# Kernel optimization log

Measured on AMD Instinct MI355X. Metric: run time of the kernel, lower is better.

The kernel has to match this reference:

```python
import jax, jax.numpy as jnp
import numpy as np

B, N, H, HID, L = 16, 256, 1024, 300, 64


def setup_inputs() -> dict:
    key = jax.random.key(0)
    ks = jax.random.split(key, 10)
    s = 0.02
    inp = {}
    inp["input"] = jax.random.normal(ks[0], (B, N, H), jnp.float32)
    # variable-length valid-token mask (first tokens always valid)
    lengths = jax.random.randint(ks[1], (B,), N // 2, N + 1)
    inp["logits_mask"] = jnp.arange(N)[None, :] < lengths[:, None]
    inp["labels"] = jax.random.randint(ks[2], (B, N, N), 0, L)
    inp["mlp_h_W"] = jax.random.normal(ks[3], (HID, H), jnp.float32) * s
    inp["mlp_h_b"] = jnp.zeros((HID,), jnp.float32)
    inp["mlp_d_W"] = jax.random.normal(ks[4], (HID, H), jnp.float32) * s
    inp["mlp_d_b"] = jnp.zeros((HID,), jnp.float32)
    # Bilinear with bias_x=bias_y=True -> weight [L, HID+1, HID+1]
    inp["bilinear_W"] = jax.random.normal(ks[5], (L, HID + 1, HID + 1), jnp.float32) * s
    inp["start_trans"] = jax.random.normal(ks[6], (L,), jnp.float32) * 0.1
    inp["trans"] = jax.random.normal(ks[7], (L, L), jnp.float32) * 0.1
    inp["end_trans"] = jax.random.normal(ks[8], (L,), jnp.float32) * 0.1
    return inp


def reference(input, logits_mask, labels, mlp_h_W, mlp_h_b, mlp_d_W, mlp_d_b,
              bilinear_W, start_trans, trans, end_trans):
    # --- biaffine scores (dropout is identity in eval) ---
    rel_h = jax.nn.relu(input @ mlp_h_W.T + mlp_h_b)            # [B,N,HID]
    rel_d = jax.nn.relu(input @ mlp_d_W.T + mlp_d_b)            # [B,N,HID]
    ones = jnp.ones((B, N, 1), rel_h.dtype)
    h1 = jnp.concatenate([rel_h, ones], -1)                     # [B,N,HID+1]
    d1 = jnp.concatenate([rel_d, ones], -1)
    # rel_atten(rel_d, rel_h) -> [B,L,Nd,Nh]; permute -> [B,Nd,Nh,L]
    s_rel = jnp.einsum('bxi,lij,byj->bxyl', d1, bilinear_W, h1)  # [B,N,N,L]

    # --- masked flatten: instead of compacting rows (data-dependent shape),
    # keep all B*N rows and weight each row's contribution by index = mask[:,0].
    # Mathematically identical to the torch compaction. ---
    s_flat = s_rel.reshape(B * N, N, L)
    emissions = jax.nn.log_softmax(s_flat, -1)                  # [M,N,L]
    crf_mask = jnp.broadcast_to(logits_mask[:, None, :], (B, N, N)).reshape(B * N, N)
    row_w = logits_mask.reshape(-1).astype(emissions.dtype)     # index = mask[:,0]
    tags = labels.reshape(B * N, N)
    mf = crf_mask.astype(emissions.dtype)

    # --- CRF numerator (vectorized, no recurrence) ---
    emit_sc = jnp.take_along_axis(emissions, tags[..., None], -1)[..., 0]  # [M,N]
    num = start_trans[tags[:, 0]] + (emit_sc * mf).sum(-1)
    num = num + (trans[tags[:, :-1], tags[:, 1:]] * mf[:, 1:]).sum(-1)
    last_idx = crf_mask.sum(-1).astype(jnp.int32) - 1
    last_tags = jnp.take_along_axis(tags, last_idx[:, None], 1)[:, 0]
    num = num + end_trans[last_tags]

    # --- CRF partition function via scan ---
    alpha0 = start_trans[None, :] + emissions[:, 0]             # [M,L]
    e_seq = emissions[:, 1:].swapaxes(0, 1)                     # [N-1,M,L]
    m_seq = crf_mask[:, 1:].swapaxes(0, 1)                      # [N-1,M]

    def fwd_step(alpha, xs):
        e_t, m_t = xs
        nxt = jax.nn.logsumexp(alpha[:, :, None] + trans[None], axis=1) + e_t
        return jnp.where(m_t[:, None], nxt, alpha), None

    alpha, _ = jax.lax.scan(fwd_step, alpha0, (e_seq, m_seq))
    den = jax.nn.logsumexp(alpha + end_trans[None, :], -1)
    loss = -((num - den) * row_w).sum()                         # reduction='sum'

    # --- Viterbi decode (padded; frozen tag repeated past seq end) ---
    ar = jnp.arange(L)

    def vit_step(score, xs):
        e_t, m_t = xs
        sc = score[:, :, None] + trans[None]                    # [M,L_prev,L_cur]
        idx = jnp.argmax(sc, axis=1)                            # [M,L]
        nxt = jnp.max(sc, axis=1) + e_t
        hist = jnp.where(m_t[:, None], idx, ar[None, :])
        return jnp.where(m_t[:, None], nxt, score), hist

    score, hist = jax.lax.scan(vit_step, alpha0, (e_seq, m_seq))
    last = jnp.argmax(score + end_trans[None, :], -1)           # [M]

    def btk(cur, h):
        prev = jnp.take_along_axis(h, cur[:, None], 1)[:, 0]
        return prev, prev

    _, rev = jax.lax.scan(btk, last, hist, reverse=True)        # [N-1,M]
    decoded = jnp.concatenate([rev.swapaxes(0, 1), last[:, None]], axis=1)  # [M,N]
    return loss, s_flat, decoded
```

## Files before the change

### kernel.cpp

```cpp
#include <hip/hip_runtime.h>
#include <math.h>


typedef short bf16x8 __attribute__((ext_vector_type(8)));
typedef float f32x4 __attribute__((ext_vector_type(4)));

__device__ __forceinline__ float rlf(float v, int l) {
    return __uint_as_float(__builtin_amdgcn_readlane(__float_as_uint(v), (unsigned)l));
}
__device__ __forceinline__ int rli(int v, int l) {
    return __builtin_amdgcn_readlane(v, (unsigned)l);
}
__device__ __forceinline__ unsigned short f2bf(float x) {
    union { float f; unsigned u; } c; c.f = x;
    unsigned r = c.u + 0x7FFF + ((c.u >> 16) & 1);
    return (unsigned short)(r >> 16);
}
__device__ __forceinline__ float bf2f(unsigned short h) {
    union { unsigned u; float f; } c; c.u = ((unsigned)h) << 16; return c.f;
}
__device__ __forceinline__ void gload16(const void* g, const void* lds) {
    __builtin_amdgcn_global_load_lds(
        (const __attribute__((address_space(1))) void*)g,
        (__attribute__((address_space(3))) void*)lds, 16, 0, 0);
}

__global__ void mask_cvt_kernel(const void* __restrict__ mraw, int* __restrict__ maskI,
                                int* __restrict__ lenB, int* __restrict__ zbuf) {
    int b = blockIdx.x, t = threadIdx.x;
    if (b == 0 && t < 8) zbuf[t] = 0;
    int i = b * 256 + t;
    unsigned int w0 = ((const unsigned int*)mraw)[0];
    int v;
    if (w0 == 1u)               v = ((const int*)mraw)[i];
    else if (w0 == 0x3F800000u) v = (((const float*)mraw)[i] != 0.f) ? 1 : 0;
    else                        v = ((const unsigned char*)mraw)[i] ? 1 : 0;
    maskI[i] = v;
    __shared__ int sh[4];
    int s = v;
    #pragma unroll
    for (int m = 32; m; m >>= 1) s += __shfl_xor(s, m);
    if ((t & 63) == 0) sh[t >> 6] = s;
    __syncthreads();
    if (t == 0) lenB[b] = sh[0] + sh[1] + sh[2] + sh[3];
}

__global__ __launch_bounds__(256)
void wsplit_kernel(const float* __restrict__ Wbil,
                   unsigned short* __restrict__ Wbh, unsigned short* __restrict__ Wbl) {
    __shared__ float Tile[304][17];
    const int l = blockIdx.x, jt = blockIdx.y, t = threadIdx.x;
    const int j0 = jt * 16;
    {
        int jj = t & 15, it = t >> 4;
        #pragma unroll
        for (int ib = 0; ib < 19; ++ib) {
            int i = ib * 16 + it;
            float v = 0.f;
            if (i < 301 && j0 + jj < 301)
                v = Wbil[(size_t)l * 90601 + (size_t)i * 301 + j0 + jj];
            Tile[i][jj] = v;
        }
    }
    __syncthreads();
    {
        int il = t & 15, jj = t >> 4;
        #pragma unroll
        for (int ib = 0; ib < 19; ++ib) {
            int i = ib * 16 + il;
            float v = Tile[i][jj];
            unsigned short hi = f2bf(v);
            unsigned short lo = f2bf(v - bf2f(hi));
            size_t o = ((size_t)(l * 304 + j0 + jj)) * 304 + i;
            Wbh[o] = hi; Wbl[o] = lo;
        }
    }
}

__global__ __launch_bounds__(256)
void mlp_kernel(const float* __restrict__ A,
                const float* __restrict__ Wh, const float* __restrict__ bh_,
                const float* __restrict__ Wd, const float* __restrict__ bd_,
                unsigned short* __restrict__ h1h, unsigned short* __restrict__ h1l,
                unsigned short* __restrict__ d1h, unsigned short* __restrict__ d1l) {
    constexpr int BM = 128, BN = 128, BK = 16;
    __shared__ float As[BK][BM + 4];
    __shared__ float Bs[BK][BN + 4];

    const int t = threadIdx.x;
    const int tn = t & 15, tm = t >> 4;
    const size_t a_row0 = (size_t)blockIdx.x * BM;
    const int n0 = blockIdx.y * BN;
    const int z = blockIdx.z;
    const float* Bm = z ? Wd : Wh;
    const float* bias = z ? bd_ : bh_;
    unsigned short* Ch = z ? d1h : h1h;
    unsigned short* Cl = z ? d1l : h1l;

    float acc[2][2][4][4] = {};
    const int ar = t >> 2, ak = (t & 3) * 4;

    for (int k0 = 0; k0 < 1024; k0 += BK) {
        {
            const float* ap = A + (a_row0 + ar) * 1024 + k0 + ak;
            float4 v0 = *(const float4*)ap;
            float4 v1 = *(const float4*)(ap + 64 * 1024);
            As[ak + 0][ar] = v0.x; As[ak + 1][ar] = v0.y;
            As[ak + 2][ar] = v0.z; As[ak + 3][ar] = v0.w;
            As[ak + 0][64 + ar] = v1.x; As[ak + 1][64 + ar] = v1.y;
            As[ak + 2][64 + ar] = v1.z; As[ak + 3][64 + ar] = v1.w;
        }
        {
            int r1 = min(n0 + ar, 299), r2 = min(n0 + 64 + ar, 299);
            const float* q1 = Bm + (size_t)r1 * 1024 + k0 + ak;
            const float* q2 = Bm + (size_t)r2 * 1024 + k0 + ak;
            float4 v0 = *(const float4*)q1;
            float4 v1 = *(const float4*)q2;
            Bs[ak + 0][ar] = v0.x; Bs[ak + 1][ar] = v0.y;
            Bs[ak + 2][ar] = v0.z; Bs[ak + 3][ar] = v0.w;
            Bs[ak + 0][64 + ar] = v1.x; Bs[ak + 1][64 + ar] = v1.y;
            Bs[ak + 2][64 + ar] = v1.z; Bs[ak + 3][64 + ar] = v1.w;
        }
        __syncthreads();
        #pragma unroll
        for (int kk = 0; kk < BK; ++kk) {
            float4 a0 = *(const float4*)&As[kk][tm * 4];
            float4 a1 = *(const float4*)&As[kk][64 + tm * 4];
            float4 b0 = *(const float4*)&Bs[kk][tn * 4];
            float4 b1 = *(const float4*)&Bs[kk][64 + tn * 4];
            float av[2][4] = {{a0.x, a0.y, a0.z, a0.w}, {a1.x, a1.y, a1.z, a1.w}};
            float bv[2][4] = {{b0.x, b0.y, b0.z, b0.w}, {b1.x, b1.y, b1.z, b1.w}};
            #pragma unroll
            for (int ih = 0; ih < 2; ++ih)
                #pragma unroll
                for (int ii = 0; ii < 4; ++ii)
                    #pragma unroll
                    for (int jh = 0; jh < 2; ++jh)
                        #pragma unroll
                        for (int jj = 0; jj < 4; ++jj)
                            acc[ih][jh][ii][jj] =
                                fmaf(av[ih][ii], bv[jh][jj], acc[ih][jh][ii][jj]);
        }
        __syncthreads();
    }

    #pragma unroll
    for (int ih = 0; ih < 2; ++ih) {
        #pragma unroll
        for (int ii = 0; ii < 4; ++ii) {
            int r = ih * 64 + tm * 4 + ii;
            #pragma unroll
            for (int jh = 0; jh < 2; ++jh) {
                int n = n0 + jh * 64 + tn * 4;
                if (n < 304) {
                    float o[4];
                    #pragma unroll
                    for (int q = 0; q < 4; ++q) {
                        int nq = n + q;
                        float v = acc[ih][jh][ii][q];
                        o[q] = (nq < 300) ? fmaxf(v + bias[min(nq, 299)], 0.f)
                                          : ((nq == 300) ? 1.f : 0.f);
                    }
                    ushort4 h4, l4;
                    h4.x = f2bf(o[0]); l4.x = f2bf(o[0] - bf2f(h4.x));
                    h4.y = f2bf(o[1]); l4.y = f2bf(o[1] - bf2f(h4.y));
                    h4.z = f2bf(o[2]); l4.z = f2bf(o[2] - bf2f(h4.z));
                    h4.w = f2bf(o[3]); l4.w = f2bf(o[3] - bf2f(h4.w));
                    size_t base = (a_row0 + r) * 304 + n;
                    *(ushort4*)&Ch[base] = h4;
                    *(ushort4*)&Cl[base] = l4;
                }
            }
        }
    }
}

template <int MODE>
__global__ __launch_bounds__(256)
void gemm_mfma(const unsigned short* __restrict__ Ah, const unsigned short* __restrict__ Al,
               const unsigned short* __restrict__ Bh, const unsigned short* __restrict__ Bl,
               float* __restrict__ outF, unsigned short* __restrict__ outUh,
               unsigned short* __restrict__ outUl, const unsigned short* __restrict__ zbuf,
               int c0) {
    __shared__ short Als[128 * 64];
    __shared__ short Bls[128 * 64];

    const int t = threadIdx.x;
    const int lane = t & 63;
    const int w = t >> 6, wr = w >> 1, wc = w & 1;
    const int bx = blockIdx.x, n0 = blockIdx.y * 128;

    int arow0;
    if constexpr (MODE == 1) {
        arow0 = c0 * 256 + bx * 128;
    } else {
        arow0 = (c0 + blockIdx.z) * 256 + bx * 128;
    }

    int kcd[4];
    size_t rowA[4], rowB[4];
    const short* ldsA[4];
    const short* ldsB[4];
    #pragma unroll
    for (int c4 = 0; c4 < 4; ++c4) {
        int ch = c4 * 256 + t;
        int r = ch >> 3;
        kcd[c4] = (ch & 7) ^ (r & 7);
        rowA[c4] = (size_t)(arow0 + r) * 304;
        if constexpr (MODE == 1) {
            rowB[c4] = (size_t)(n0 + r) * 304;
        } else {
            int rb = n0 + r;
            rowB[c4] = (size_t)(blockIdx.z * 256 + (rb >> 6)) * 19456 +
                       (size_t)(rb & 63) * 304;
        }
        int wavebase = (c4 * 256 + (t & ~63)) * 8;
        ldsA[c4] = &Als[wavebase];
        ldsB[c4] = &Bls[wavebase];
    }

    f32x4 acc[4][4];
    #pragma unroll
    for (int i = 0; i < 4; ++i)
        #pragma unroll
        for (int j = 0; j < 4; ++j)
            acc[i][j] = (f32x4){0.f, 0.f, 0.f, 0.f};

    const int rowA_l = wr * 64 + (lane & 15);
    const int rowB_l = wc * 64 + (lane & 15);
    const int csub = lane >> 4;
    const int cxor = lane & 7;

    for (int it = 0; it < 15; ++it) {
        const int it8 = it * 8;
        #pragma unroll
        for (int c4 = 0; c4 < 4; ++c4) {
            int kg = it8 + kcd[c4];
            {
                const unsigned short* sa;
                if (kg < 38)       sa = Ah + rowA[c4] + (size_t)kg * 8;
                else if (kg < 76)  sa = Al + rowA[c4] + (size_t)(kg - 38) * 8;
                else if (kg < 114) sa = Ah + rowA[c4] + (size_t)(kg - 76) * 8;
                else               sa = zbuf;
                gload16(sa, ldsA[c4]);
            }
            {
                const unsigned short* sb;
                if (kg < 38)       sb = Bh + rowB[c4] + (size_t)kg * 8;
                else if (kg < 76)  sb = Bh + rowB[c4] + (size_t)(kg - 38) * 8;
                else if (kg < 114) sb = Bl + rowB[c4] + (size_t)(kg - 76) * 8;
                else               sb = zbuf;
                gload16(sb, ldsB[c4]);
            }
        }
        __syncthreads();

        #pragma unroll
        for (int kh = 0; kh < 2; ++kh) {
            const int kcr = ((kh * 4 + csub) ^ cxor) * 8;
            bf16x8 af[4], bfr[4];
            #pragma unroll
            for (int f = 0; f < 4; ++f)
                af[f] = *(const bf16x8*)&Als[(rowA_l + f * 16) * 64 + kcr];
            #pragma unroll
            for (int f = 0; f < 4; ++f)
                bfr[f] = *(const bf16x8*)&Bls[(rowB_l + f * 16) * 64 + kcr];
            #pragma unroll
            for (int fr = 0; fr < 4; ++fr)
                #pragma unroll
                for (int fb = 0; fb < 4; ++fb)
                    acc[fr][fb] = __builtin_amdgcn_mfma_f32_16x16x32_bf16(
                        af[fr], bfr[fb], acc[fr][fb], 0, 0, 0);
        }
        __syncthreads();
    }

    const int mbase = bx * 128 + wr * 64 + ((lane >> 4) << 2);
    const int nbase = n0 + wc * 64 + (lane & 15);
    #pragma unroll
    for (int fb = 0; fb < 4; ++fb) {
        const int n = nbase + fb * 16;
        if constexpr (MODE == 1) {
            #pragma unroll
            for (int fr = 0; fr < 4; ++fr) {
                #pragma unroll
                for (int reg = 0; reg < 4; ++reg) {
                    int xloc = mbase + fr * 16 + reg;
                    float v = acc[fr][fb][reg];
                    unsigned short hi = f2bf(v);
                    unsigned short lo = f2bf(v - bf2f(hi));
                    size_t o = (size_t)xloc * 19456 + n;
                    outUh[o] = hi;
                    outUl[o] = lo;
                }
            }
        } else {
            const int xx = n >> 6, lt = n & 63;
            const size_t sbase = (size_t)(c0 + blockIdx.z) * 4194304 +
                                 (size_t)xx * 16384 + lt;
            #pragma unroll
            for (int fr = 0; fr < 4; ++fr) {
                #pragma unroll
                for (int reg = 0; reg < 4; ++reg) {
                    int y = mbase + fr * 16 + reg;
                    outF[sbase + (size_t)y * 64] = acc[fr][fb][reg];
                }
            }
        }
    }
}

__global__ __launch_bounds__(256, 4)
void fwd_kernel(const float* __restrict__ s_flat, const int* __restrict__ lenB,
                const int* __restrict__ maskI, const int* __restrict__ labels,
                const float* __restrict__ trans, const float* __restrict__ start_trans,
                const float* __restrict__ end_trans, float* __restrict__ rowterm) {
    __shared__ float T[4096];
    const int t = threadIdx.x;
    for (int i = t; i < 4096; i += 256) T[i] = trans[i];
    __syncthreads();

    const int lane = t & 63, wid = t >> 6;
    const int row = blockIdx.x * 4 + wid;
    if (maskI[row] == 0) {
        if (lane == 0) rowterm[row] = 0.f;
        return;
    }
    const int b = row >> 8;
    const int len = lenB[b];
    const float* srow = s_flat + (size_t)row * 16384;
    const int* lrow = labels + (size_t)row * 256;

    float Ec[64];
    #pragma unroll
    for (int p = 0; p < 64; ++p) Ec[p] = __expf(T[p * 64 + lane]);

    const float et = end_trans[lane];

    float sv = srow[lane];
    int tagprev = lrow[0];
    float num = start_trans[tagprev] + rlf(sv, tagprev);
    float alpha = start_trans[lane] + sv;

    float sv_pre = srow[64 + lane];

    for (int y = 1; y < len; ++y) {
        sv = sv_pre;
        int ynext = (y + 1 < len) ? (y + 1) : (len - 1);
        sv_pre = srow[ynext * 64 + lane];

        const int tag = lrow[y];
        num += rlf(sv, tag) + T[tagprev * 64 + tag];
        tagprev = tag;

        float am = alpha;
        #pragma unroll
        for (int m = 32; m; m >>= 1) am = fmaxf(am, __shfl_xor(am, m));
        float ea = __expf(alpha - am);
        float a0 = 0.f, a1 = 0.f, a2 = 0.f, a3 = 0.f;
        #pragma unroll
        for (int p = 0; p < 64; p += 4) {
            a0 = fmaf(rlf(ea, p + 0), Ec[p + 0], a0);
            a1 = fmaf(rlf(ea, p + 1), Ec[p + 1], a1);
            a2 = fmaf(rlf(ea, p + 2), Ec[p + 2], a2);
            a3 = fmaf(rlf(ea, p + 3), Ec[p + 3], a3);
        }
        alpha = am + __logf((a0 + a1) + (a2 + a3)) + sv;
    }

    num += end_trans[tagprev];

    float da = alpha + et;
    float dmx = da;
    #pragma unroll
    for (int m = 32; m; m >>= 1) dmx = fmaxf(dmx, __shfl_xor(dmx, m));
    float ds = __expf(da - dmx);
    #pragma unroll
    for (int m = 32; m; m >>= 1) ds += __shfl_xor(ds, m);
    float den = dmx + __logf(ds);

    if (lane == 0) rowterm[row] = num - den;
}

__global__ __launch_bounds__(256, 4)
void vitf_kernel(const float* __restrict__ s_flat, const int* __restrict__ lenB,
                 const float* __restrict__ trans, const float* __restrict__ start_trans,
                 const float* __restrict__ end_trans, float* __restrict__ vsb,
                 float* __restrict__ decoded) {
    const int t = threadIdx.x;
    const int lane = t & 63, wid = t >> 6;
    const int row = blockIdx.x * 4 + wid;
    const int len = lenB[row >> 8];
    const float* srow = s_flat + (size_t)row * 16384;
    float* vrow = vsb + (size_t)row * 16384;

    float sv = srow[lane];
    float vs = start_trans[lane] + sv;
    float sv_pre = srow[64 + lane];

    for (int y = 1; y < len; ++y) {
        vrow[(y - 1) * 64 + lane] = vs;
        float svc = sv_pre;
        int ynext = (y + 1 < len) ? (y + 1) : (len - 1);
        sv_pre = srow[ynext * 64 + lane];

        float m0 = -3.4e38f, m1 = -3.4e38f, m2 = -3.4e38f, m3 = -3.4e38f;
        #pragma unroll
        for (int p = 0; p < 64; p += 8) {
            float t0 = rlf(vs, p + 0) + trans[(p + 0) * 64 + lane];
            float t1 = rlf(vs, p + 1) + trans[(p + 1) * 64 + lane];
            m0 = fmaxf(fmaxf(t0, t1), m0);
            float t2 = rlf(vs, p + 2) + trans[(p + 2) * 64 + lane];
            float t3 = rlf(vs, p + 3) + trans[(p + 3) * 64 + lane];
            m1 = fmaxf(fmaxf(t2, t3), m1);
            float t4 = rlf(vs, p + 4) + trans[(p + 4) * 64 + lane];
            float t5 = rlf(vs, p + 5) + trans[(p + 5) * 64 + lane];
            m2 = fmaxf(fmaxf(t4, t5), m2);
            float t6 = rlf(vs, p + 6) + trans[(p + 6) * 64 + lane];
            float t7 = rlf(vs, p + 7) + trans[(p + 7) * 64 + lane];
            m3 = fmaxf(fmaxf(t6, t7), m3);
        }
        vs = fmaxf(fmaxf(m0, m1), fmaxf(m2, m3)) + svc;
    }

    float fe = vs + end_trans[lane];
    float mx = fe;
    #pragma unroll
    for (int m = 32; m; m >>= 1) mx = fmaxf(mx, __shfl_xor(mx, m));
    unsigned long long msk = __ballot(fe == mx);
    int fi = (int)__builtin_ctzll(msk);

    if (lane == 0) decoded[(size_t)row * 256 + 255] = (float)fi;
}

__global__ __launch_bounds__(256)
void vitb_kernel(const float* __restrict__ vsb, const int* __restrict__ lenB,
                 const float* __restrict__ trans, float* __restrict__ decoded) {
    __shared__ float Tt[64][65];
    const int t = threadIdx.x;
    for (int i = t; i < 4096; i += 256) {
        int p = i >> 6, c = i & 63;
        Tt[c][p] = trans[i];
    }
    __syncthreads();

    const int lane = t & 63, wid = t >> 6;
    const int row = blockIdx.x * 4 + wid;
    const int len = lenB[row >> 8];
    const float* vrow = vsb + (size_t)row * 16384;
    float* drow = decoded + (size_t)row * 256;

    int cur = (int)drow[255];

    for (int y = len - 1 + lane; y < 255; y += 64) drow[y] = (float)cur;

    float v0 = vrow[(len - 2) * 64 + lane];
    float v1 = (len >= 3) ? vrow[(len - 3) * 64 + lane] : 0.f;

    for (int y = len - 2; y >= 0; --y) {
        float vy = v0;
        v0 = v1;
        v1 = (y >= 2) ? vrow[(y - 2) * 64 + lane] : 0.f;

        float tp = vy + Tt[cur][lane];
        float mx = tp;
        #pragma unroll
        for (int m = 32; m; m >>= 1) mx = fmaxf(mx, __shfl_xor(mx, m));
        unsigned long long msk = __ballot(tp == mx);
        cur = (int)__builtin_ctzll(msk);
        if (lane == 0) drow[y] = (float)cur;
    }
}

__global__ __launch_bounds__(256, 3)
void vit_kernel(const float* __restrict__ s_flat, const int* __restrict__ lenB,
                const float* __restrict__ trans, const float* __restrict__ start_trans,
                const float* __restrict__ end_trans, unsigned char* __restrict__ hist,
                float* __restrict__ decoded) {
    const int t = threadIdx.x;
    const int lane = t & 63, wid = t >> 6;
    const int row = blockIdx.x * 4 + wid;
    const int len = lenB[row >> 8];
    const float* srow = s_flat + (size_t)row * 16384;
    unsigned char* hrow = hist + (size_t)row * 16320;

    float sv = srow[lane];
    float vs = start_trans[lane] + sv;
    float sv_pre = srow[64 + lane];

    for (int y = 1; y < len; ++y) {
        sv = sv_pre;
        int ynext = (y + 1 < len) ? (y + 1) : (len - 1);
        sv_pre = srow[ynext * 64 + lane];

        float b0 = -3.4e38f, b1 = -3.4e38f, b2 = -3.4e38f, b3 = -3.4e38f;
        int i0 = 0, i1 = 1, i2 = 2, i3 = 3;
        #pragma unroll
        for (int p = 0; p < 64; p += 4) {
            float t0 = rlf(vs, p + 0) + trans[(p + 0) * 64 + lane]; if (t0 > b0) { b0 = t0; i0 = p + 0; }
            float t1 = rlf(vs, p + 1) + trans[(p + 1) * 64 + lane]; if (t1 > b1) { b1 = t1; i1 = p + 1; }
            float t2 = rlf(vs, p + 2) + trans[(p + 2) * 64 + lane]; if (t2 > b2) { b2 = t2; i2 = p + 2; }
            float t3 = rlf(vs, p + 3) + trans[(p + 3) * 64 + lane]; if (t3 > b3) { b3 = t3; i3 = p + 3; }
        }
        bool c;
        c = (b1 > b0) || (b1 == b0 && i1 < i0);
        float bA = c ? b1 : b0; int iA = c ? i1 : i0;
        c = (b3 > b2) || (b3 == b2 && i3 < i2);
        float bB = c ? b3 : b2; int iB = c ? i3 : i2;
        c = (bB > bA) || (bB == bA && iB < iA);
        float bbv = c ? bB : bA; int bi = c ? iB : iA;

        hrow[(size_t)(y - 1) * 64 + lane] = (unsigned char)bi;
        vs = bbv + sv;
    }

    float fv = vs + end_trans[lane]; int fi = lane;
    #pragma unroll
    for (int m = 32; m; m >>= 1) {
        float ov = __shfl_xor(fv, m);
        int oi = __shfl_xor(fi, m);
        bool cc = (ov > fv) || (ov == fv && oi < fi);
        fv = cc ? ov : fv; fi = cc ? oi : fi;
    }

    if (lane == 0) decoded[(size_t)row * 256 + 255] = (float)fi;
}

__global__ __launch_bounds__(256)
void backtrack_kernel(const unsigned char* __restrict__ hist, const int* __restrict__ lenB,
                      float* __restrict__ decoded) {
    const int lane = threadIdx.x & 63, wid = threadIdx.x >> 6;
    const int row = blockIdx.x * 4 + wid;
    const int len = lenB[row >> 8];
    const unsigned char* hrow = hist + (size_t)row * 16320;
    float* drow = decoded + (size_t)row * 256;

    int cur = (int)drow[255];
    for (int y = len - 1 + lane; y < 255; y += 64) drow[y] = (float)cur;

    int t0 = len - 2;
    int c0 = (int)hrow[(t0 - 0) * 64 + lane];
    int c1 = (int)hrow[(t0 - 1) * 64 + lane];
    int c2 = (int)hrow[(t0 - 2) * 64 + lane];
    int c3 = (int)hrow[(t0 - 3) * 64 + lane];

    for (int y = t0; y >= 0; y -= 4) {
        int yn = y - 4;
        int n0 = 0, n1 = 0, n2 = 0, n3 = 0;
        if (yn - 0 >= 0) n0 = (int)hrow[(yn - 0) * 64 + lane];
        if (yn - 1 >= 0) n1 = (int)hrow[(yn - 1) * 64 + lane];
        if (yn - 2 >= 0) n2 = (int)hrow[(yn - 2) * 64 + lane];
        if (yn - 3 >= 0) n3 = (int)hrow[(yn - 3) * 64 + lane];

        cur = rli(c0, cur);
        if (lane == 0) drow[y] = (float)cur;
        if (y - 1 >= 0) { cur = rli(c1, cur); if (lane == 0) drow[y - 1] = (float)cur; }
        if (y - 2 >= 0) { cur = rli(c2, cur); if (lane == 0) drow[y - 2] = (float)cur; }
        if (y - 3 >= 0) { cur = rli(c3, cur); if (lane == 0) drow[y - 3] = (float)cur; }

        c0 = n0; c1 = n1; c2 = n2; c3 = n3;
    }
}

__global__ void loss_kernel(const float* __restrict__ rowterm, float* __restrict__ out) {
    __shared__ float wsum[4];
    int t = threadIdx.x;
    float s = 0.f;
    for (int i = t; i < 4096; i += 256) s += rowterm[i];
    #pragma unroll
    for (int m = 32; m; m >>= 1) s += __shfl_xor(s, m);
    if ((t & 63) == 0) wsum[t >> 6] = s;
    __syncthreads();
    if (t == 0) out[0] = -(wsum[0] + wsum[1] + wsum[2] + wsum[3]);
}

extern "C" void kernel_launch(void* const* d_in, const int* in_sizes, int n_in,
                              void* d_out, int out_size, void* d_ws, size_t ws_size,
                              hipStream_t stream) {
    const float* input  = (const float*)d_in[0];
    const void*  mraw   = d_in[1];
    const int*   labels = (const int*)d_in[2];
    const float* Wh_in  = (const float*)d_in[3];
    const float* bh     = (const float*)d_in[4];
    const float* Wd_in  = (const float*)d_in[5];
    const float* bd     = (const float*)d_in[6];
    const float* Wbil   = (const float*)d_in[7];
    const float* stt    = (const float*)d_in[8];
    const float* trans  = (const float*)d_in[9];
    const float* ett    = (const float*)d_in[10];

    float* out     = (float*)d_out;
    float* s_flat  = out + 1;
    float* decoded = out + 1 + (size_t)67108864;

    char* ws = (char*)d_ws;
    size_t off = 0;
    unsigned short* h1h = (unsigned short*)(ws + off); off += (size_t)4096 * 304 * 2;
    unsigned short* h1l = (unsigned short*)(ws + off); off += (size_t)4096 * 304 * 2;
    unsigned short* d1h = (unsigned short*)(ws + off); off += (size_t)4096 * 304 * 2;
    unsigned short* d1l = (unsigned short*)(ws + off); off += (size_t)4096 * 304 * 2;
    unsigned short* Wbh = (unsigned short*)(ws + off); off += (size_t)19456 * 304 * 2;
    unsigned short* Wbl = (unsigned short*)(ws + off); off += (size_t)19456 * 304 * 2;
    int* maskI = (int*)(ws + off); off += 16384;
    int* lenB  = (int*)(ws + off); off += 256;
    int* zbuf  = (int*)(ws + off); off += 256;
    float* rowterm = (float*)(ws + off); off += 16384;

    const size_t vsb_bytes = (size_t)4096 * 16384 * 4;
    const size_t hist_bytes = (size_t)4096 * 16320;
    const size_t perb = (size_t)256 * 19456 * 2 * 2;

    bool newpath = (ws_size >= off + vsb_bytes + perb);
    float* vsb = nullptr;
    unsigned char* hist = nullptr;
    if (newpath) { vsb  = (float*)(ws + off); off += vsb_bytes; }
    else         { hist = (unsigned char*)(ws + off); off += hist_bytes; }

    unsigned short* Uh = (unsigned short*)(ws + off);
    size_t avail = (ws_size > off) ? ws_size - off : 0;
    int CB = (int)(avail / perb);
    if (CB < 1) CB = 1;
    if (CB > 16) CB = 16;
    unsigned short* Ul = Uh + (size_t)CB * 256 * 19456;

    mask_cvt_kernel<<<16, 256, 0, stream>>>(mraw, maskI, lenB, zbuf);
    wsplit_kernel<<<dim3(64, 19), 256, 0, stream>>>(Wbil, Wbh, Wbl);
    mlp_kernel<<<dim3(32, 3, 2), 256, 0, stream>>>(input, Wh_in, bh, Wd_in, bd,
                                                   h1h, h1l, d1h, d1l);

    for (int c0 = 0; c0 < 16; c0 += CB) {
        int cb = (CB < 16 - c0) ? CB : (16 - c0);
        gemm_mfma<1><<<dim3(cb * 2, 152), 256, 0, stream>>>(
            d1h, d1l, Wbh, Wbl, nullptr, Uh, Ul, (const unsigned short*)zbuf, c0);
        gemm_mfma<2><<<dim3(2, 128, cb), 256, 0, stream>>>(
            h1h, h1l, Uh, Ul, s_flat, nullptr, nullptr, (const unsigned short*)zbuf, c0);
    }

    fwd_kernel<<<1024, 256, 0, stream>>>(s_flat, lenB, maskI, labels, trans, stt, ett,
                                         rowterm);
    if (newpath) {
        vitf_kernel<<<1024, 256, 0, stream>>>(s_flat, lenB, trans, stt, ett, vsb, decoded);
        vitb_kernel<<<1024, 256, 0, stream>>>(vsb, lenB, trans, decoded);
    } else {
        vit_kernel<<<1024, 256, 0, stream>>>(s_flat, lenB, trans, stt, ett, hist, decoded);
        backtrack_kernel<<<1024, 256, 0, stream>>>(hist, lenB, decoded);
    }
    loss_kernel<<<1, 256, 0, stream>>>(rowterm, out);
}
```

Baseline: 1.334 ms.

## Fuse CRF forward and Viterbi forward into one kernel; cap GEMM chunk batch

Merges the CRF forward (log-partition plus gold-path score) pass and the Viterbi forward pass into a single kernel, so each row's emission scores are read from s_flat once instead of twice and one launch is removed. Masked rows still run the Viterbi recurrence but skip the forward-algorithm work. It also caps the number of batch chunks per GEMM launch at 4 instead of 16, which changes how the bilinear GEMMs are staged through the workspace. The fused kernel carries more live registers (the Ec table plus the Viterbi state), which may lower occupancy, and the two serial recurrences now run back to back in one wave.

```diff
diff --git a/kernel.cpp b/kernel.cpp
--- a/kernel.cpp
+++ b/kernel.cpp
@@ -311,10 +311,11 @@
 }
 
 __global__ __launch_bounds__(256, 4)
-void fwd_kernel(const float* __restrict__ s_flat, const int* __restrict__ lenB,
-                const int* __restrict__ maskI, const int* __restrict__ labels,
-                const float* __restrict__ trans, const float* __restrict__ start_trans,
-                const float* __restrict__ end_trans, float* __restrict__ rowterm) {
+void crffv_kernel(const float* __restrict__ s_flat, const int* __restrict__ lenB,
+                  const int* __restrict__ maskI, const int* __restrict__ labels,
+                  const float* __restrict__ trans, const float* __restrict__ start_trans,
+                  const float* __restrict__ end_trans, float* __restrict__ rowterm,
+                  float* __restrict__ vsb, float* __restrict__ decoded) {
     __shared__ float T[4096];
     const int t = threadIdx.x;
     for (int i = t; i < 4096; i += 256) T[i] = trans[i];
@@ -322,14 +323,11 @@
 
     const int lane = t & 63, wid = t >> 6;
     const int row = blockIdx.x * 4 + wid;
-    if (maskI[row] == 0) {
-        if (lane == 0) rowterm[row] = 0.f;
-        return;
-    }
-    const int b = row >> 8;
-    const int len = lenB[b];
+    const int len = lenB[row >> 8];
+    const bool doFwd = (maskI[row] != 0);
     const float* srow = s_flat + (size_t)row * 16384;
     const int* lrow = labels + (size_t)row * 256;
+    float* vrow = vsb + (size_t)row * 16384;
 
     float Ec[64];
     #pragma unroll
@@ -341,6 +339,7 @@
     int tagprev = lrow[0];
     float num = start_trans[tagprev] + rlf(sv, tagprev);
     float alpha = start_trans[lane] + sv;
+    float vs = alpha;
 
     float sv_pre = srow[64 + lane];
 
@@ -349,61 +348,7 @@
         int ynext = (y + 1 < len) ? (y + 1) : (len - 1);
         sv_pre = srow[ynext * 64 + lane];
 
-        const int tag = lrow[y];
-        num += rlf(sv, tag) + T[tagprev * 64 + tag];
-        tagprev = tag;
-
-        float am = alpha;
-        #pragma unroll
-        for (int m = 32; m; m >>= 1) am = fmaxf(am, __shfl_xor(am, m));
-        float ea = __expf(alpha - am);
-        float a0 = 0.f, a1 = 0.f, a2 = 0.f, a3 = 0.f;
-        #pragma unroll
-        for (int p = 0; p < 64; p += 4) {
-            a0 = fmaf(rlf(ea, p + 0), Ec[p + 0], a0);
-            a1 = fmaf(rlf(ea, p + 1), Ec[p + 1], a1);
-            a2 = fmaf(rlf(ea, p + 2), Ec[p + 2], a2);
-            a3 = fmaf(rlf(ea, p + 3), Ec[p + 3], a3);
-        }
-        alpha = am + __logf((a0 + a1) + (a2 + a3)) + sv;
-    }
-
-    num += end_trans[tagprev];
-
-    float da = alpha + et;
-    float dmx = da;
-    #pragma unroll
-    for (int m = 32; m; m >>= 1) dmx = fmaxf(dmx, __shfl_xor(dmx, m));
-    float ds = __expf(da - dmx);
-    #pragma unroll
-    for (int m = 32; m; m >>= 1) ds += __shfl_xor(ds, m);
-    float den = dmx + __logf(ds);
-
-    if (lane == 0) rowterm[row] = num - den;
-}
-
-__global__ __launch_bounds__(256, 4)
-void vitf_kernel(const float* __restrict__ s_flat, const int* __restrict__ lenB,
-                 const float* __restrict__ trans, const float* __restrict__ start_trans,
-                 const float* __restrict__ end_trans, float* __restrict__ vsb,
-                 float* __restrict__ decoded) {
-    const int t = threadIdx.x;
-    const int lane = t & 63, wid = t >> 6;
-    const int row = blockIdx.x * 4 + wid;
-    const int len = lenB[row >> 8];
-    const float* srow = s_flat + (size_t)row * 16384;
-    float* vrow = vsb + (size_t)row * 16384;
-
-    float sv = srow[lane];
-    float vs = start_trans[lane] + sv;
-    float sv_pre = srow[64 + lane];
-
-    for (int y = 1; y < len; ++y) {
         vrow[(y - 1) * 64 + lane] = vs;
-        float svc = sv_pre;
-        int ynext = (y + 1 < len) ? (y + 1) : (len - 1);
-        sv_pre = srow[ynext * 64 + lane];
-
         float m0 = -3.4e38f, m1 = -3.4e38f, m2 = -3.4e38f, m3 = -3.4e38f;
         #pragma unroll
         for (int p = 0; p < 64; p += 8) {
@@ -420,17 +365,52 @@
             float t7 = rlf(vs, p + 7) + trans[(p + 7) * 64 + lane];
             m3 = fmaxf(fmaxf(t6, t7), m3);
         }
-        vs = fmaxf(fmaxf(m0, m1), fmaxf(m2, m3)) + svc;
-    }
-
-    float fe = vs + end_trans[lane];
+        float vsn = fmaxf(fmaxf(m0, m1), fmaxf(m2, m3)) + sv;
+
+        if (doFwd) {
+            const int tag = lrow[y];
+            num += rlf(sv, tag) + T[tagprev * 64 + tag];
+            tagprev = tag;
+
+            float am = alpha;
+            #pragma unroll
+            for (int m = 32; m; m >>= 1) am = fmaxf(am, __shfl_xor(am, m));
+            float ea = __expf(alpha - am);
+            float a0 = 0.f, a1 = 0.f, a2 = 0.f, a3 = 0.f;
+            #pragma unroll
+            for (int p = 0; p < 64; p += 4) {
+                a0 = fmaf(rlf(ea, p + 0), Ec[p + 0], a0);
+                a1 = fmaf(rlf(ea, p + 1), Ec[p + 1], a1);
+                a2 = fmaf(rlf(ea, p + 2), Ec[p + 2], a2);
+                a3 = fmaf(rlf(ea, p + 3), Ec[p + 3], a3);
+            }
+            alpha = am + __logf((a0 + a1) + (a2 + a3)) + sv;
+        }
+        vs = vsn;
+    }
+
+    float fe = vs + et;
     float mx = fe;
     #pragma unroll
     for (int m = 32; m; m >>= 1) mx = fmaxf(mx, __shfl_xor(mx, m));
     unsigned long long msk = __ballot(fe == mx);
     int fi = (int)__builtin_ctzll(msk);
-
     if (lane == 0) decoded[(size_t)row * 256 + 255] = (float)fi;
+
+    if (doFwd) {
+        num += end_trans[tagprev];
+        float da = alpha + et;
+        float dmx = da;
+        #pragma unroll
+        for (int m = 32; m; m >>= 1) dmx = fmaxf(dmx, __shfl_xor(dmx, m));
+        float ds = __expf(da - dmx);
+        #pragma unroll
+        for (int m = 32; m; m >>= 1) ds += __shfl_xor(ds, m);
+        float den = dmx + __logf(ds);
+        if (lane == 0) rowterm[row] = num - den;
+    } else {
+        if (lane == 0) rowterm[row] = 0.f;
+    }
 }
 
 __global__ __launch_bounds__(256)
@@ -470,6 +450,74 @@
         cur = (int)__builtin_ctzll(msk);
         if (lane == 0) drow[y] = (float)cur;
     }
+}
+
+__global__ __launch_bounds__(256, 4)
+void fwd_kernel(const float* __restrict__ s_flat, const int* __restrict__ lenB,
+                const int* __restrict__ maskI, const int* __restrict__ labels,
+                const float* __restrict__ trans, const float* __restrict__ start_trans,
+                const float* __restrict__ end_trans, float* __restrict__ rowterm) {
+    __shared__ float T[4096];
+    const int t = threadIdx.x;
+    for (int i = t; i < 4096; i += 256) T[i] = trans[i];
+    __syncthreads();
+
+    const int lane = t & 63, wid = t >> 6;
+    const int row = blockIdx.x * 4 + wid;
+    if (maskI[row] == 0) {
+        if (lane == 0) rowterm[row] = 0.f;
+        return;
+    }
+    const int len = lenB[row >> 8];
+    const float* srow = s_flat + (size_t)row * 16384;
+    const int* lrow = labels + (size_t)row * 256;
+
+    float Ec[64];
+    #pragma unroll
+    for (int p = 0; p < 64; ++p) Ec[p] = __expf(T[p * 64 + lane]);
+
+    const float et = end_trans[lane];
+
+    float sv = srow[lane];
+    int tagprev = lrow[0];
+    float num = start_trans[tagprev] + rlf(sv, tagprev);
+    float alpha = start_trans[lane] + sv;
+    float sv_pre = srow[64 + lane];
+
+    for (int y = 1; y < len; ++y) {
+        sv = sv_pre;
+        int ynext = (y + 1 < len) ? (y + 1) : (len - 1);
+        sv_pre = srow[ynext * 64 + lane];
+
+        const int tag = lrow[y];
+        num += rlf(sv, tag) + T[tagprev * 64 + tag];
+        tagprev = tag;
+
+        float am = alpha;
+        #pragma unroll
+        for (int m = 32; m; m >>= 1) am = fmaxf(am, __shfl_xor(am, m));
+        float ea = __expf(alpha - am);
+        float a0 = 0.f, a1 = 0.f, a2 = 0.f, a3 = 0.f;
+        #pragma unroll
+        for (int p = 0; p < 64; p += 4) {
+            a0 = fmaf(rlf(ea, p + 0), Ec[p + 0], a0);
+            a1 = fmaf(rlf(ea, p + 1), Ec[p + 1], a1);
+            a2 = fmaf(rlf(ea, p + 2), Ec[p + 2], a2);
+            a3 = fmaf(rlf(ea, p + 3), Ec[p + 3], a3);
+        }
+        alpha = am + __logf((a0 + a1) + (a2 + a3)) + sv;
+    }
+
+    num += end_trans[tagprev];
+    float da = alpha + et;
+    float dmx = da;
+    #pragma unroll
+    for (int m = 32; m; m >>= 1) dmx = fmaxf(dmx, __shfl_xor(dmx, m));
+    float ds = __expf(da - dmx);
+    #pragma unroll
+    for (int m = 32; m; m >>= 1) ds += __shfl_xor(ds, m);
+    float den = dmx + __logf(ds);
+    if (lane == 0) rowterm[row] = num - den;
 }
 
 __global__ __launch_bounds__(256, 3)
@@ -620,7 +668,7 @@
     size_t avail = (ws_size > off) ? ws_size - off : 0;
     int CB = (int)(avail / perb);
     if (CB < 1) CB = 1;
-    if (CB > 16) CB = 16;
+    if (CB > 4) CB = 4;
     unsigned short* Ul = Uh + (size_t)CB * 256 * 19456;
 
     mask_cvt_kernel<<<16, 256, 0, stream>>>(mraw, maskI, lenB, zbuf);
@@ -636,12 +684,13 @@
             h1h, h1l, Uh, Ul, s_flat, nullptr, nullptr, (const unsigned short*)zbuf, c0);
     }
 
-    fwd_kernel<<<1024, 256, 0, stream>>>(s_flat, lenB, maskI, labels, trans, stt, ett,
-                                         rowterm);
     if (newpath) {
-        vitf_kernel<<<1024, 256, 0, stream>>>(s_flat, lenB, trans, stt, ett, vsb, decoded);
+        crffv_kernel<<<1024, 256, 0, stream>>>(s_flat, lenB, maskI, labels, trans,
+                                               stt, ett, rowterm, vsb, decoded);
         vitb_kernel<<<1024, 256, 0, stream>>>(vsb, lenB, trans, decoded);
     } else {
+        fwd_kernel<<<1024, 256, 0, stream>>>(s_flat, lenB, maskI, labels, trans,
+                                             stt, ett, rowterm);
         vit_kernel<<<1024, 256, 0, stream>>>(s_flat, lenB, trans, stt, ett, hist, decoded);
         backtrack_kernel<<<1024, 256, 0, stream>>>(hist, lenB, decoded);
     }
```

Measured after the change: 1.899 ms. 1.42x slower.
